# Optimization experiments

Measured on AMD Instinct MI355X. Metric: run time of the kernel, lower is better.

Reference implementation:

```python
import jax, jax.numpy as jnp
import numpy as np

FG_THRESH = 0.5

def _descriptors(fmap, scribbles):
    # fmap: [B, C, h, w]; scribbles: [B, I, H, W]
    B, C, h, w = fmap.shape
    I = scribbles.shape[1]
    # bilinear resize (align_corners=False == half-pixel, no antialias, like torch)
    sr = jax.image.resize(scribbles, (B, I, h, w), method='bilinear', antialias=False)
    mask = (sr > FG_THRESH).astype(fmap.dtype)                 # [B, I, h, w]
    cnt = mask.sum(axis=(-1, -2))                              # [B, I]
    ssum = jnp.einsum('bihw,bchw->bic', mask, fmap)            # masked sum over HW
    mean = ssum / jnp.maximum(cnt, 1.0)[..., None]             # [B, I, C]
    # fallback when a mask has no foreground pixels: feature at argmax of soft mask
    idx = jnp.argmax(sr.reshape(B, I, h * w), axis=-1)         # [B, I]
    fflat = fmap.reshape(B, C, h * w)
    fb = jnp.take_along_axis(fflat, idx[:, None, :], axis=2)   # [B, C, I]
    fb = fb.transpose(0, 2, 1)                                 # [B, I, C]
    return jnp.where((cnt > 0)[..., None], mean, fb)

def setup_inputs() -> dict:
    key = jax.random.key(0)
    k0, k1, k2, k3 = jax.random.split(key, 4)
    return {
        'feat0': jax.random.normal(k0, (8, 256, 128, 128), dtype=jnp.float32),
        'feat1': jax.random.normal(k1, (8, 256, 64, 64), dtype=jnp.float32),
        'feat2': jax.random.normal(k2, (8, 256, 32, 32), dtype=jnp.float32),
        'scribbles': jax.random.uniform(k3, (8, 16, 512, 512), dtype=jnp.float32),
    }

def reference(feat0, feat1, feat2, scribbles):
    # multi_scale=True, random_bg_queries=False: per-level masked mean pool,
    # then average descriptors across feature levels. Output: [B, I, C]
    d0 = _descriptors(feat0, scribbles)
    d1 = _descriptors(feat1, scribbles)
    d2 = _descriptors(feat2, scribbles)
    return (d0 + d1 + d2) / 3.0
```

## Files before the change

### kernel.cpp

```cpp
#include <hip/hip_runtime.h>
#include <stdint.h>

#define NB 8
#define NI 16
#define NC 256
#define SH 512

typedef __bf16 bf16x8 __attribute__((ext_vector_type(8)));
typedef float f32x4 __attribute__((ext_vector_type(4)));
typedef uint32_t u32x4 __attribute__((ext_vector_type(4)));

static const size_t OFF_M0   = 0;
static const size_t OFF_M1   = OFF_M0 + (size_t)NB * 16384 * 2;
static const size_t OFF_M2   = OFF_M1 + (size_t)NB * 4096 * 2;
static const size_t OFF_CNT  = OFF_M2 + (size_t)NB * 1024 * 2;
static const size_t OFF_ARG  = OFF_CNT + (size_t)3 * NB * NI * 4;
static const size_t OFF_SSUM = OFF_ARG + (size_t)3 * NB * NI * 8;
static const size_t WS_NEED  = OFF_SSUM + (size_t)3 * NB * NI * NC * 4;

__device__ __forceinline__ float4 ld4(const float* p) {
    return *reinterpret_cast<const float4*>(p);
}

__device__ __forceinline__ uint32_t bf16pk(float lo, float hi) {
    uint32_t u0 = __float_as_uint(lo), u1 = __float_as_uint(hi);
    uint32_t h0 = (u0 + 0x7FFFu + ((u0 >> 16) & 1u)) >> 16;
    uint32_t h1 = (u1 + 0x7FFFu + ((u1 >> 16) & 1u)) >> 16;
    return h0 | (h1 << 16);
}

template<int W, int S>
__device__ __forceinline__ void mask_level(const float* __restrict__ scr,
                                           uint16_t* __restrict__ mask,
                                           unsigned long long* __restrict__ argm,
                                           int b, int bx, int tid, int* lcnt) {
    const int P = W * W;
    const int pix = bx * 256 + tid;
    const int y = pix / W;
    const int x = pix - y * W;
    const int r0 = S * y + (S / 2 - 1);
    const int c0 = S * x + (S / 2 - 1);
    const int lane = tid & 63;
    const float* sb = scr + (size_t)b * NI * SH * SH + (size_t)r0 * SH;
    unsigned int mword = 0;
    for (int i = 0; i < NI; ++i) {
        const float* sp = sb + (size_t)i * SH * SH;
        float s4;
        if constexpr (S == 4) {
            float4 q0 = ld4(sp + (c0 - 1));
            float4 q1 = ld4(sp + SH + (c0 - 1));
            s4 = (q0.y + q0.z) + (q1.y + q1.z);
        } else {
            s4 = (sp[c0] + sp[c0 + 1]) + (sp[SH + c0] + sp[SH + c0 + 1]);
        }
        float sr = 0.25f * s4;
        bool bit = sr > 0.5f;
        mword |= bit ? (1u << i) : 0u;
        unsigned long long bal = __ballot(bit);
        if (lane == 0) atomicAdd(&lcnt[i], (int)__popcll(bal));
        if (bal == 0ull) {
            unsigned int srb = __float_as_uint(sr);
            unsigned int mx = srb;
            #pragma unroll
            for (int off = 1; off < 64; off <<= 1) {
                unsigned int o = __shfl_xor(mx, off, 64);
                mx = (o > mx) ? o : mx;
            }
            unsigned long long win = __ballot(srb == mx);
            if (lane == 0) {
                int wl = __ffsll(win) - 1;
                unsigned int wpix = (unsigned int)(bx * 256 + (tid & ~63) + wl);
                unsigned long long key = (((unsigned long long)mx) << 32)
                                       | (unsigned long long)(0xFFFFFFFFu - wpix);
                atomicMax(&argm[b * NI + i], key);
            }
        }
    }
    mask[(size_t)b * P + pix] = (uint16_t)mword;
}

__global__ __launch_bounds__(256) void mask_all(const float* __restrict__ scr,
                                                uint16_t* __restrict__ m0,
                                                uint16_t* __restrict__ m1,
                                                uint16_t* __restrict__ m2,
                                                int* __restrict__ cnt,
                                                unsigned long long* __restrict__ argm) {
    __shared__ int lcnt[NI];
    const int tid = threadIdx.x;
    const int b = blockIdx.y;
    const int bx = blockIdx.x;
    if (tid < NI) lcnt[tid] = 0;
    __syncthreads();
    int lvl;
    if (bx < 64) {
        mask_level<128, 4>(scr, m0, argm + 0 * NB * NI, b, bx, tid, lcnt);
        lvl = 0;
    } else if (bx < 80) {
        mask_level<64, 8>(scr, m1, argm + 1 * NB * NI, b, bx - 64, tid, lcnt);
        lvl = 1;
    } else {
        mask_level<32, 16>(scr, m2, argm + 2 * NB * NI, b, bx - 80, tid, lcnt);
        lvl = 2;
    }
    __syncthreads();
    if (tid < NI) {
        int v = lcnt[tid];
        if (v) atomicAdd(&cnt[lvl * NB * NI + b * NI + tid], v);
    }
}

template<int P>
__device__ __forceinline__ void ssum_level(const float* __restrict__ f,
                                           const uint16_t* __restrict__ m,
                                           float* __restrict__ ssum_l,
                                           int b, int chunk, int tid) {
    const int wave = tid >> 6;
    const int lane = tid & 63;
    const int kg = lane >> 4;
    const int cl = lane & 15;
    const int c0 = wave * 64;
    const int kb = chunk * 256;
    const uint16_t* mp = m + (size_t)b * P + kb + kg * 8;
    const float* fp0 = f + ((size_t)b * NC + c0 + cl) * P + kb + kg * 8;
    f32x4 acc0 = {0.f, 0.f, 0.f, 0.f};
    f32x4 acc1 = {0.f, 0.f, 0.f, 0.f};
    f32x4 acc2 = {0.f, 0.f, 0.f, 0.f};
    f32x4 acc3 = {0.f, 0.f, 0.f, 0.f};
    for (int ks = 0; ks < 8; ++ks) {
        const uint4 wA = *reinterpret_cast<const uint4*>(mp + ks * 32);
        u32x4 au;
        au.x = ((wA.x >> cl) & 0x10001u) * 0x3F80u;
        au.y = ((wA.y >> cl) & 0x10001u) * 0x3F80u;
        au.z = ((wA.z >> cl) & 0x10001u) * 0x3F80u;
        au.w = ((wA.w >> cl) & 0x10001u) * 0x3F80u;
        const bf16x8 av = __builtin_bit_cast(bf16x8, au);
        const float* fk = fp0 + ks * 32;
        #pragma unroll
        for (int nt = 0; nt < 4; ++nt) {
            const float* fr = fk + (size_t)nt * 16 * P;
            float4 v0 = ld4(fr);
            float4 v1 = ld4(fr + 4);
            u32x4 bu;
            bu.x = bf16pk(v0.x, v0.y);
            bu.y = bf16pk(v0.z, v0.w);
            bu.z = bf16pk(v1.x, v1.y);
            bu.w = bf16pk(v1.z, v1.w);
            const bf16x8 bv = __builtin_bit_cast(bf16x8, bu);
            if (nt == 0) acc0 = __builtin_amdgcn_mfma_f32_16x16x32_bf16(av, bv, acc0, 0, 0, 0);
            if (nt == 1) acc1 = __builtin_amdgcn_mfma_f32_16x16x32_bf16(av, bv, acc1, 0, 0, 0);
            if (nt == 2) acc2 = __builtin_amdgcn_mfma_f32_16x16x32_bf16(av, bv, acc2, 0, 0, 0);
            if (nt == 3) acc3 = __builtin_amdgcn_mfma_f32_16x16x32_bf16(av, bv, acc3, 0, 0, 0);
        }
    }
    float* sb = ssum_l + (size_t)b * NI * NC;
    #pragma unroll
    for (int nt = 0; nt < 4; ++nt) {
        const f32x4 ac = (nt == 0) ? acc0 : (nt == 1) ? acc1 : (nt == 2) ? acc2 : acc3;
        const int c = c0 + nt * 16 + cl;
        #pragma unroll
        for (int r = 0; r < 4; ++r)
            atomicAdd(&sb[(kg * 4 + r) * NC + c], ac[r]);
    }
}

__global__ __launch_bounds__(256) void ssum_all(const float* __restrict__ f0,
                                                const float* __restrict__ f1,
                                                const float* __restrict__ f2,
                                                const uint16_t* __restrict__ m0,
                                                const uint16_t* __restrict__ m1,
                                                const uint16_t* __restrict__ m2,
                                                float* __restrict__ ssum) {
    const int tid = threadIdx.x;
    const int b = blockIdx.y;
    const int bx = blockIdx.x;
    if (bx < 64) {
        ssum_level<16384>(f0, m0, ssum + (size_t)0 * NB * NI * NC, b, bx, tid);
    } else if (bx < 80) {
        ssum_level<4096>(f1, m1, ssum + (size_t)1 * NB * NI * NC, b, bx - 64, tid);
    } else {
        ssum_level<1024>(f2, m2, ssum + (size_t)2 * NB * NI * NC, b, bx - 80, tid);
    }
}

__global__ void final_kernel(const float* __restrict__ f0,
                             const float* __restrict__ f1,
                             const float* __restrict__ f2,
                             const int* __restrict__ cnt,
                             const unsigned long long* __restrict__ argm,
                             const float* __restrict__ ssum,
                             float* __restrict__ out) {
    const int bi = blockIdx.x;
    const int c = threadIdx.x;
    const int b = bi >> 4;
    const float* fl[3] = { f0, f1, f2 };
    const int Ps[3] = { 16384, 4096, 1024 };
    float r = 0.0f;
    #pragma unroll
    for (int l = 0; l < 3; ++l) {
        int cn = cnt[l * NB * NI + bi];
        float v;
        if (cn > 0) {
            v = ssum[((size_t)l * NB * NI + bi) * NC + c] / (float)cn;
        } else {
            unsigned int p = 0xFFFFFFFFu -
                (unsigned int)(argm[l * NB * NI + bi] & 0xFFFFFFFFull);
            v = fl[l][((size_t)b * NC + c) * Ps[l] + p];
        }
        r += v;
    }
    out[(size_t)bi * NC + c] = r * (1.0f / 3.0f);
}

extern "C" void kernel_launch(void* const* d_in, const int* in_sizes, int n_in,
                              void* d_out, int out_size, void* d_ws, size_t ws_size,
                              hipStream_t stream) {
    const float* f0  = (const float*)d_in[0];
    const float* f1  = (const float*)d_in[1];
    const float* f2  = (const float*)d_in[2];
    const float* scr = (const float*)d_in[3];
    float* out = (float*)d_out;
    char* ws = (char*)d_ws;
    if (ws_size < WS_NEED) return;

    uint16_t* m0 = (uint16_t*)(ws + OFF_M0);
    uint16_t* m1 = (uint16_t*)(ws + OFF_M1);
    uint16_t* m2 = (uint16_t*)(ws + OFF_M2);
    int* cnt = (int*)(ws + OFF_CNT);
    unsigned long long* argm = (unsigned long long*)(ws + OFF_ARG);
    float* ssum = (float*)(ws + OFF_SSUM);

    hipMemsetAsync(ws + OFF_CNT, 0, WS_NEED - OFF_CNT, stream);

    mask_all<<<dim3(84, NB), 256, 0, stream>>>(scr, m0, m1, m2, cnt, argm);

    ssum_all<<<dim3(84, NB), 256, 0, stream>>>(f0, f1, f2, m0, m1, m2, ssum);

    final_kernel<<<NB * NI, NC, 0, stream>>>(f0, f1, f2, cnt, argm, ssum, out);
}
```

Baseline: 70.80 us.

## Fuse mask and masked-sum kernels, replace atomics with per-chunk partials

Merges the mask-building and MFMA masked-sum kernels into one, so each block computes its 256-pixel mask chunk in shared memory and uses it at once, with no global mask round trip. Global atomics for counts, argmax keys and sums are replaced by per-chunk partial slots that the final kernel reduces, which also removes the memset. Costs: a larger partial-sum workspace, and the final kernel now loops over up to 64 partials per output. The bf16 conversion also switches to compiler casts.

```diff
diff --git a/kernel.cpp b/kernel.cpp
--- a/kernel.cpp
+++ b/kernel.cpp
@@ -5,41 +5,36 @@
 #define NI 16
 #define NC 256
 #define SH 512
+#define NCH 84
 
 typedef __bf16 bf16x8 __attribute__((ext_vector_type(8)));
 typedef float f32x4 __attribute__((ext_vector_type(4)));
 typedef uint32_t u32x4 __attribute__((ext_vector_type(4)));
 
-static const size_t OFF_M0   = 0;
-static const size_t OFF_M1   = OFF_M0 + (size_t)NB * 16384 * 2;
-static const size_t OFF_M2   = OFF_M1 + (size_t)NB * 4096 * 2;
-static const size_t OFF_CNT  = OFF_M2 + (size_t)NB * 1024 * 2;
-static const size_t OFF_ARG  = OFF_CNT + (size_t)3 * NB * NI * 4;
-static const size_t OFF_SSUM = OFF_ARG + (size_t)3 * NB * NI * 8;
-static const size_t WS_NEED  = OFF_SSUM + (size_t)3 * NB * NI * NC * 4;
+static const size_t OFF_SSP = 0;
+static const size_t OFF_CNT = OFF_SSP + (size_t)NB * NCH * NI * NC * 4;
+static const size_t OFF_KEY = OFF_CNT + (size_t)NB * NCH * NI * 4;
+static const size_t WS_NEED = OFF_KEY + (size_t)NB * NCH * NI * 8;
 
 __device__ __forceinline__ float4 ld4(const float* p) {
     return *reinterpret_cast<const float4*>(p);
 }
 
-__device__ __forceinline__ uint32_t bf16pk(float lo, float hi) {
-    uint32_t u0 = __float_as_uint(lo), u1 = __float_as_uint(hi);
-    uint32_t h0 = (u0 + 0x7FFFu + ((u0 >> 16) & 1u)) >> 16;
-    uint32_t h1 = (u1 + 0x7FFFu + ((u1 >> 16) & 1u)) >> 16;
-    return h0 | (h1 << 16);
-}
-
-template<int W, int S>
-__device__ __forceinline__ void mask_level(const float* __restrict__ scr,
-                                           uint16_t* __restrict__ mask,
-                                           unsigned long long* __restrict__ argm,
-                                           int b, int bx, int tid, int* lcnt) {
-    const int P = W * W;
-    const int pix = bx * 256 + tid;
+template<int W, int S, int P>
+__device__ __forceinline__ void do_chunk(const float* __restrict__ f,
+                                         const float* __restrict__ scr,
+                                         float* __restrict__ ssp,
+                                         int* __restrict__ cntp,
+                                         unsigned long long* __restrict__ keyp,
+                                         int b, int chunk, int slot, int tid,
+                                         uint16_t* __restrict__ lmask,
+                                         int* __restrict__ lcnt,
+                                         unsigned long long* __restrict__ lkey) {
+    const int pix = chunk * 256 + tid;
     const int y = pix / W;
     const int x = pix - y * W;
     const int r0 = S * y + (S / 2 - 1);
-    const int c0 = S * x + (S / 2 - 1);
+    const int c0s = S * x + (S / 2 - 1);
     const int lane = tid & 63;
     const float* sb = scr + (size_t)b * NI * SH * SH + (size_t)r0 * SH;
     unsigned int mword = 0;
@@ -47,19 +42,18 @@
         const float* sp = sb + (size_t)i * SH * SH;
         float s4;
         if constexpr (S == 4) {
-            float4 q0 = ld4(sp + (c0 - 1));
-            float4 q1 = ld4(sp + SH + (c0 - 1));
+            float4 q0 = ld4(sp + (c0s - 1));
+            float4 q1 = ld4(sp + SH + (c0s - 1));
             s4 = (q0.y + q0.z) + (q1.y + q1.z);
         } else {
-            s4 = (sp[c0] + sp[c0 + 1]) + (sp[SH + c0] + sp[SH + c0 + 1]);
-        }
-        float sr = 0.25f * s4;
-        bool bit = sr > 0.5f;
+            s4 = (sp[c0s] + sp[c0s + 1]) + (sp[SH + c0s] + sp[SH + c0s + 1]);
+        }
+        bool bit = s4 > 2.0f;
         mword |= bit ? (1u << i) : 0u;
         unsigned long long bal = __ballot(bit);
         if (lane == 0) atomicAdd(&lcnt[i], (int)__popcll(bal));
         if (bal == 0ull) {
-            unsigned int srb = __float_as_uint(sr);
+            unsigned int srb = __float_as_uint(0.25f * s4);
             unsigned int mx = srb;
             #pragma unroll
             for (int off = 1; off < 64; off <<= 1) {
@@ -68,66 +62,35 @@
             }
             unsigned long long win = __ballot(srb == mx);
             if (lane == 0) {
-                int wl = __ffsll(win) - 1;
-                unsigned int wpix = (unsigned int)(bx * 256 + (tid & ~63) + wl);
+                int wl = __ffsll((unsigned long long)win) - 1;
+                unsigned int wpix = (unsigned int)(chunk * 256 + (tid & ~63) + wl);
                 unsigned long long key = (((unsigned long long)mx) << 32)
                                        | (unsigned long long)(0xFFFFFFFFu - wpix);
-                atomicMax(&argm[b * NI + i], key);
-            }
-        }
-    }
-    mask[(size_t)b * P + pix] = (uint16_t)mword;
-}
-
-__global__ __launch_bounds__(256) void mask_all(const float* __restrict__ scr,
-                                                uint16_t* __restrict__ m0,
-                                                uint16_t* __restrict__ m1,
-                                                uint16_t* __restrict__ m2,
-                                                int* __restrict__ cnt,
-                                                unsigned long long* __restrict__ argm) {
-    __shared__ int lcnt[NI];
-    const int tid = threadIdx.x;
-    const int b = blockIdx.y;
-    const int bx = blockIdx.x;
-    if (tid < NI) lcnt[tid] = 0;
-    __syncthreads();
-    int lvl;
-    if (bx < 64) {
-        mask_level<128, 4>(scr, m0, argm + 0 * NB * NI, b, bx, tid, lcnt);
-        lvl = 0;
-    } else if (bx < 80) {
-        mask_level<64, 8>(scr, m1, argm + 1 * NB * NI, b, bx - 64, tid, lcnt);
-        lvl = 1;
-    } else {
-        mask_level<32, 16>(scr, m2, argm + 2 * NB * NI, b, bx - 80, tid, lcnt);
-        lvl = 2;
-    }
+                atomicMax(&lkey[i], key);
+            }
+        }
+    }
+    lmask[tid] = (uint16_t)mword;
     __syncthreads();
     if (tid < NI) {
-        int v = lcnt[tid];
-        if (v) atomicAdd(&cnt[lvl * NB * NI + b * NI + tid], v);
-    }
-}
-
-template<int P>
-__device__ __forceinline__ void ssum_level(const float* __restrict__ f,
-                                           const uint16_t* __restrict__ m,
-                                           float* __restrict__ ssum_l,
-                                           int b, int chunk, int tid) {
+        cntp[slot * NI + tid] = lcnt[tid];
+        keyp[slot * NI + tid] = lkey[tid];
+    }
+
     const int wave = tid >> 6;
-    const int lane = tid & 63;
     const int kg = lane >> 4;
     const int cl = lane & 15;
     const int c0 = wave * 64;
     const int kb = chunk * 256;
-    const uint16_t* mp = m + (size_t)b * P + kb + kg * 8;
+    const uint16_t* lmp = lmask + kg * 8;
     const float* fp0 = f + ((size_t)b * NC + c0 + cl) * P + kb + kg * 8;
     f32x4 acc0 = {0.f, 0.f, 0.f, 0.f};
     f32x4 acc1 = {0.f, 0.f, 0.f, 0.f};
     f32x4 acc2 = {0.f, 0.f, 0.f, 0.f};
     f32x4 acc3 = {0.f, 0.f, 0.f, 0.f};
+    #pragma unroll
     for (int ks = 0; ks < 8; ++ks) {
-        const uint4 wA = *reinterpret_cast<const uint4*>(mp + ks * 32);
+        const uint4 wA = *reinterpret_cast<const uint4*>(lmp + ks * 32);
         u32x4 au;
         au.x = ((wA.x >> cl) & 0x10001u) * 0x3F80u;
         au.y = ((wA.y >> cl) & 0x10001u) * 0x3F80u;
@@ -137,78 +100,111 @@
         const float* fk = fp0 + ks * 32;
         #pragma unroll
         for (int nt = 0; nt < 4; ++nt) {
-            const float* fr = fk + (size_t)nt * 16 * P;
+            const float* fr = fk + (size_t)(nt * 16) * P;
             float4 v0 = ld4(fr);
             float4 v1 = ld4(fr + 4);
-            u32x4 bu;
-            bu.x = bf16pk(v0.x, v0.y);
-            bu.y = bf16pk(v0.z, v0.w);
-            bu.z = bf16pk(v1.x, v1.y);
-            bu.w = bf16pk(v1.z, v1.w);
-            const bf16x8 bv = __builtin_bit_cast(bf16x8, bu);
+            bf16x8 bv;
+            bv[0] = (__bf16)v0.x; bv[1] = (__bf16)v0.y;
+            bv[2] = (__bf16)v0.z; bv[3] = (__bf16)v0.w;
+            bv[4] = (__bf16)v1.x; bv[5] = (__bf16)v1.y;
+            bv[6] = (__bf16)v1.z; bv[7] = (__bf16)v1.w;
             if (nt == 0) acc0 = __builtin_amdgcn_mfma_f32_16x16x32_bf16(av, bv, acc0, 0, 0, 0);
             if (nt == 1) acc1 = __builtin_amdgcn_mfma_f32_16x16x32_bf16(av, bv, acc1, 0, 0, 0);
             if (nt == 2) acc2 = __builtin_amdgcn_mfma_f32_16x16x32_bf16(av, bv, acc2, 0, 0, 0);
             if (nt == 3) acc3 = __builtin_amdgcn_mfma_f32_16x16x32_bf16(av, bv, acc3, 0, 0, 0);
         }
     }
-    float* sb = ssum_l + (size_t)b * NI * NC;
+    float* sb2 = ssp + (size_t)slot * (NI * NC);
     #pragma unroll
     for (int nt = 0; nt < 4; ++nt) {
         const f32x4 ac = (nt == 0) ? acc0 : (nt == 1) ? acc1 : (nt == 2) ? acc2 : acc3;
         const int c = c0 + nt * 16 + cl;
         #pragma unroll
         for (int r = 0; r < 4; ++r)
-            atomicAdd(&sb[(kg * 4 + r) * NC + c], ac[r]);
-    }
-}
-
-__global__ __launch_bounds__(256) void ssum_all(const float* __restrict__ f0,
-                                                const float* __restrict__ f1,
-                                                const float* __restrict__ f2,
-                                                const uint16_t* __restrict__ m0,
-                                                const uint16_t* __restrict__ m1,
-                                                const uint16_t* __restrict__ m2,
-                                                float* __restrict__ ssum) {
+            sb2[(kg * 4 + r) * NC + c] = ac[r];
+    }
+}
+
+__global__ __launch_bounds__(256) void fused_kernel(const float* __restrict__ f0,
+                                                    const float* __restrict__ f1,
+                                                    const float* __restrict__ f2,
+                                                    const float* __restrict__ scr,
+                                                    float* __restrict__ ssp,
+                                                    int* __restrict__ cntp,
+                                                    unsigned long long* __restrict__ keyp) {
+    __shared__ __align__(16) uint16_t lmask[256];
+    __shared__ int lcnt[NI];
+    __shared__ unsigned long long lkey[NI];
     const int tid = threadIdx.x;
     const int b = blockIdx.y;
     const int bx = blockIdx.x;
+    if (tid < NI) { lcnt[tid] = 0; lkey[tid] = 0ull; }
+    __syncthreads();
+    const int slot = b * NCH + bx;
     if (bx < 64) {
-        ssum_level<16384>(f0, m0, ssum + (size_t)0 * NB * NI * NC, b, bx, tid);
+        do_chunk<128, 4, 16384>(f0, scr, ssp, cntp, keyp, b, bx, slot, tid, lmask, lcnt, lkey);
     } else if (bx < 80) {
-        ssum_level<4096>(f1, m1, ssum + (size_t)1 * NB * NI * NC, b, bx - 64, tid);
+        do_chunk<64, 8, 4096>(f1, scr, ssp, cntp, keyp, b, bx - 64, slot, tid, lmask, lcnt, lkey);
     } else {
-        ssum_level<1024>(f2, m2, ssum + (size_t)2 * NB * NI * NC, b, bx - 80, tid);
-    }
-}
-
-__global__ void final_kernel(const float* __restrict__ f0,
-                             const float* __restrict__ f1,
-                             const float* __restrict__ f2,
-                             const int* __restrict__ cnt,
-                             const unsigned long long* __restrict__ argm,
-                             const float* __restrict__ ssum,
-                             float* __restrict__ out) {
+        do_chunk<32, 16, 1024>(f2, scr, ssp, cntp, keyp, b, bx - 80, slot, tid, lmask, lcnt, lkey);
+    }
+}
+
+__global__ __launch_bounds__(256) void final_kernel(const float* __restrict__ f0,
+                                                    const float* __restrict__ f1,
+                                                    const float* __restrict__ f2,
+                                                    const int* __restrict__ cntp,
+                                                    const unsigned long long* __restrict__ keyp,
+                                                    const float* __restrict__ ssp,
+                                                    float* __restrict__ out) {
+    __shared__ int scnt[3];
+    __shared__ unsigned long long skey[3];
     const int bi = blockIdx.x;
-    const int c = threadIdx.x;
     const int b = bi >> 4;
-    const float* fl[3] = { f0, f1, f2 };
-    const int Ps[3] = { 16384, 4096, 1024 };
-    float r = 0.0f;
+    const int i = bi & 15;
+    const int tid = threadIdx.x;
+    const int CH[3] = {64, 16, 4};
+    const int O[3] = {0, 64, 80};
+    if (tid < 64) {
+        #pragma unroll
+        for (int l = 0; l < 3; ++l) {
+            int v = 0;
+            unsigned long long k = 0ull;
+            if (tid < CH[l]) {
+                const int slot = b * NCH + O[l] + tid;
+                v = cntp[slot * NI + i];
+                k = keyp[slot * NI + i];
+            }
+            #pragma unroll
+            for (int off = 32; off > 0; off >>= 1) {
+                v += __shfl_down(v, off, 64);
+                unsigned long long ko = __shfl_down(k, off, 64);
+                k = (ko > k) ? ko : k;
+            }
+            if (tid == 0) { scnt[l] = v; skey[l] = k; }
+        }
+    }
+    __syncthreads();
+    const float* fl[3] = {f0, f1, f2};
+    const int Ps[3] = {16384, 4096, 1024};
+    const int c = tid;
+    float r = 0.f;
     #pragma unroll
     for (int l = 0; l < 3; ++l) {
-        int cn = cnt[l * NB * NI + bi];
+        const int cn = scnt[l];
         float v;
         if (cn > 0) {
-            v = ssum[((size_t)l * NB * NI + bi) * NC + c] / (float)cn;
+            float s = 0.f;
+            for (int j = 0; j < CH[l]; ++j)
+                s += ssp[((size_t)(b * NCH + O[l] + j) * NI + i) * NC + c];
+            v = s / (float)cn;
         } else {
-            unsigned int p = 0xFFFFFFFFu -
-                (unsigned int)(argm[l * NB * NI + bi] & 0xFFFFFFFFull);
+            unsigned int p = 0xFFFFFFFFu - (unsigned int)(skey[l] & 0xFFFFFFFFull);
             v = fl[l][((size_t)b * NC + c) * Ps[l] + p];
         }
         r += v;
     }
-    out[(size_t)bi * NC + c] = r * (1.0f / 3.0f);
+    out[(size_t)bi * NC + c] = r * (1.f / 3.f);
 }
 
 extern "C" void kernel_launch(void* const* d_in, const int* in_sizes, int n_in,
@@ -222,18 +218,10 @@
     char* ws = (char*)d_ws;
     if (ws_size < WS_NEED) return;
 
-    uint16_t* m0 = (uint16_t*)(ws + OFF_M0);
-    uint16_t* m1 = (uint16_t*)(ws + OFF_M1);
-    uint16_t* m2 = (uint16_t*)(ws + OFF_M2);
-    int* cnt = (int*)(ws + OFF_CNT);
-    unsigned long long* argm = (unsigned long long*)(ws + OFF_ARG);
-    float* ssum = (float*)(ws + OFF_SSUM);
-
-    hipMemsetAsync(ws + OFF_CNT, 0, WS_NEED - OFF_CNT, stream);
-
-    mask_all<<<dim3(84, NB), 256, 0, stream>>>(scr, m0, m1, m2, cnt, argm);
-
-    ssum_all<<<dim3(84, NB), 256, 0, stream>>>(f0, f1, f2, m0, m1, m2, ssum);
-
-    final_kernel<<<NB * NI, NC, 0, stream>>>(f0, f1, f2, cnt, argm, ssum, out);
-}
+    float* ssp = (float*)(ws + OFF_SSP);
+    int* cntp = (int*)(ws + OFF_CNT);
+    unsigned long long* keyp = (unsigned long long*)(ws + OFF_KEY);
+
+    fused_kernel<<<dim3(NCH, NB), 256, 0, stream>>>(f0, f1, f2, scr, ssp, cntp, keyp);
+    final_kernel<<<NB * NI, NC, 0, stream>>>(f0, f1, f2, cntp, keyp, ssp, out);
+}
```

Result: faster. 65.13 us (-8.0%).
